# Kernel optimization log

Hardware: AMD Instinct MI355X
Metric: run time of the kernel (lower is better)

## Reference

```python
import jax, jax.numpy as jnp
import numpy as np

H, HK, D = 16, 4, 128          # query heads, kv heads, head_dim
HID, INTER = 2048, 8192        # hidden_size, intermediate_size
L, N_UND = 4096, 3072          # total packed len (sum(sample_lens)), num und tokens
SAMPLE_LENS = [2048, 2048]
EPS = 1e-6


def rmsnorm(x, w, eps=EPS):
    v = jnp.mean(jnp.square(x), axis=-1, keepdims=True)
    return x * jax.lax.rsqrt(v + eps) * w


def setup_inputs() -> dict:
    key = jax.random.key(0)
    ks = jax.random.split(key, 12)
    x = jax.random.normal(ks[0], (N_UND, HID), jnp.float32)
    und_idx = jnp.sort(jax.random.permutation(ks[1], L)[:N_UND]).astype(jnp.int64)
    # RoPE tables (source computes RoPE but its attention consumes pre-RoPE tensors)
    pos = jnp.arange(L, dtype=jnp.float32)
    inv_freq = 1.0 / (10000.0 ** (jnp.arange(0, D, 2, dtype=jnp.float32) / D))
    ang = pos[:, None] * inv_freq[None, :]
    cos = jnp.concatenate([jnp.cos(ang), jnp.cos(ang)], axis=-1)
    sin = jnp.concatenate([jnp.sin(ang), jnp.sin(ang)], axis=-1)
    # block-diagonal causal mask over packed sequence (one causal block per sample)
    offs = np.cumsum([0] + SAMPLE_LENS)
    m = np.zeros((L, L), dtype=bool)
    for a, b in zip(offs[:-1], offs[1:]):
        m[a:b, a:b] = np.tril(np.ones((b - a, b - a), dtype=bool))
    mask = jnp.asarray(m)
    w = lambda k, shape: jax.random.normal(k, shape, jnp.float32) * 0.02
    return dict(
        packed_sequence=x, und_idx=und_idx, cos=cos, sin=sin, mask=mask,
        Wq=w(ks[2], (H * D, HID)), bq=w(ks[3], (H * D,)),
        Wk=w(ks[4], (HK * D, HID)), bk=w(ks[5], (HK * D,)),
        Wv=w(ks[6], (HK * D, HID)), bv=w(ks[7], (HK * D,)),
        Wo=w(ks[8], (HID, H * D)),
        q_norm_w=jnp.ones((D,), jnp.float32), k_norm_w=jnp.ones((D,), jnp.float32),
        ln1_w=jnp.ones((HID,), jnp.float32), ln2_w=jnp.ones((HID,), jnp.float32),
        Wg=w(ks[9], (INTER, HID)), Wu=w(ks[10], (INTER, HID)), Wd=w(ks[11], (HID, INTER)),
    )


def reference(packed_sequence, und_idx, cos, sin, mask, Wq, bq, Wk, bk, Wv, bv, Wo,
              q_norm_w, k_norm_w, ln1_w, ln2_w, Wg, Wu, Wd):
    G = H // HK  # num_key_value_groups
    resid = packed_sequence
    x = rmsnorm(packed_sequence, ln1_w)
    # projections on und tokens only, then scatter into zero-initialized packed tensors
    q = (x @ Wq.T + bq).reshape(-1, H, D)
    k = (x @ Wk.T + bk).reshape(-1, HK, D)
    v = (x @ Wv.T + bv).reshape(-1, HK, D)
    Q = jnp.zeros((L, H, D), x.dtype).at[und_idx].set(q)
    K = jnp.zeros((L, HK, D), x.dtype).at[und_idx].set(k)
    V = jnp.zeros((L, HK, D), x.dtype).at[und_idx].set(v)
    # QK RMSNorm (zero rows stay zero, matching scatter-of-normed-und-rows)
    Q = rmsnorm(Q, q_norm_w)
    K = rmsnorm(K, k_norm_w)
    # NOTE: the source applies apply_rotary_pos_emb(Q, K, cos, sin) but both attention
    # branches consume the pre-RoPE normed tensors, so RoPE has no effect; we mirror that.
    Kx = jnp.repeat(K, G, axis=1)  # [L, H, D] GQA expand (each kv head repeated G times)
    Vx = jnp.repeat(V, G, axis=1)
    scores = jnp.einsum('qhd,khd->hqk', Q, Kx) / jnp.sqrt(jnp.asarray(D, x.dtype))
    scores = jnp.where(mask[None], scores, jnp.finfo(scores.dtype).min)
    attn = jax.nn.softmax(scores, axis=-1)
    ctx = jnp.einsum('hqk,khd->qhd', attn, Vx).reshape(L, H * D)
    attn_out = ctx[und_idx] @ Wo.T
    h = resid + attn_out
    y = rmsnorm(h, ln2_w)
    mlp = (jax.nn.silu(y @ Wg.T) * (y @ Wu.T)) @ Wd.T
    return h + mlp
```

## Files before the change

kernel.cpp:

```cpp
#include <hip/hip_runtime.h>
#include <math.h>


#define NU     3072
#define LPACK  4096
#define HIDN   2048
#define QKV_LD 3072
#define EPSF   1e-6f

typedef unsigned short u16;
typedef unsigned int   u32;
typedef __attribute__((ext_vector_type(8)))  __bf16 bf16x8;
typedef __attribute__((ext_vector_type(4)))  float  f32x4;
typedef __attribute__((ext_vector_type(16))) float  f32x16;

union FRAG { uint4 q; u16 u[8]; bf16x8 b; };

__device__ __forceinline__ u16 f2bf(float f) {
    u32 u = __float_as_uint(f);
    u32 r = (u + 0x7fffu + ((u >> 16) & 1u)) >> 16;
    return (u16)r;
}
__device__ __forceinline__ float bf2f(u16 h) {
    return __uint_as_float(((u32)h) << 16);
}
__device__ __forceinline__ void gload_lds16(const u16* g, u16* lds) {
    __builtin_amdgcn_global_load_lds(
        (const __attribute__((address_space(1))) u32*)g,
        (__attribute__((address_space(3))) u32*)lds, 16, 0, 0);
}


__global__ __launch_bounds__(256) void inv_init_kernel(int* __restrict__ inv) {
    inv[blockIdx.x * 256 + threadIdx.x] = -1;
}
__global__ __launch_bounds__(256) void inv_set_kernel(const int* __restrict__ und,
                                                      int* __restrict__ inv) {
    int i = blockIdx.x * 256 + threadIdx.x;
    inv[und[i]] = i;
}


struct CvtArgs {
    const float* src[7];
    u16*         dst[7];
    int          n8[7];
};

__global__ __launch_bounds__(256) void cvt_all_kernel(CvtArgs a) {
    int seg = blockIdx.y;
    const float* in = a.src[seg];
    u16* out = a.dst[seg];
    int n8 = a.n8[seg];
    int idx = blockIdx.x * 256 + threadIdx.x;
    int stride = gridDim.x * 256;
    for (int i = idx; i < n8; i += stride) {
        float4 va = *(const float4*)(in + (size_t)i * 8);
        float4 vb = *(const float4*)(in + (size_t)i * 8 + 4);
        FRAG f;
        f.u[0] = f2bf(va.x); f.u[1] = f2bf(va.y); f.u[2] = f2bf(va.z); f.u[3] = f2bf(va.w);
        f.u[4] = f2bf(vb.x); f.u[5] = f2bf(vb.y); f.u[6] = f2bf(vb.z); f.u[7] = f2bf(vb.w);
        *(uint4*)(out + (size_t)i * 8) = f.q;
    }
}


__global__ __launch_bounds__(256) void rmsnorm_bf16_kernel(const float* __restrict__ in,
                                                           const float* __restrict__ w,
                                                           u16* __restrict__ out) {
    int row = blockIdx.x;
    const float4* p = (const float4*)(in + (size_t)row * HIDN);
    float4 a = p[threadIdx.x * 2];
    float4 b = p[threadIdx.x * 2 + 1];
    float ss = a.x*a.x + a.y*a.y + a.z*a.z + a.w*a.w
             + b.x*b.x + b.y*b.y + b.z*b.z + b.w*b.w;
    #pragma unroll
    for (int off = 32; off > 0; off >>= 1) ss += __shfl_xor(ss, off, 64);
    __shared__ float red[4];
    if ((threadIdx.x & 63) == 0) red[threadIdx.x >> 6] = ss;
    __syncthreads();
    float tot = red[0] + red[1] + red[2] + red[3];
    float sc  = rsqrtf(tot * (1.0f / HIDN) + EPSF);
    const float4* wp = (const float4*)w;
    float4 w0 = wp[threadIdx.x * 2], w1 = wp[threadIdx.x * 2 + 1];
    FRAG f;
    f.u[0] = f2bf(a.x*sc*w0.x); f.u[1] = f2bf(a.y*sc*w0.y);
    f.u[2] = f2bf(a.z*sc*w0.z); f.u[3] = f2bf(a.w*sc*w0.w);
    f.u[4] = f2bf(b.x*sc*w1.x); f.u[5] = f2bf(b.y*sc*w1.y);
    f.u[6] = f2bf(b.z*sc*w1.z); f.u[7] = f2bf(b.w*sc*w1.w);
    *(uint4*)(out + (size_t)row * HIDN + threadIdx.x * 8) = f.q;
}


__global__ __launch_bounds__(64) void qnorm_kernel(u16* __restrict__ qkv,
                                                   const float* __restrict__ w) {
    int i = blockIdx.x, h = blockIdx.y, t = threadIdx.x;
    u16* p = qkv + (size_t)i * QKV_LD + h * 128 + t * 2;
    u32 pr = *(u32*)p;
    float x0 = bf2f((u16)(pr & 0xffff)), x1 = bf2f((u16)(pr >> 16));
    float ss = x0*x0 + x1*x1;
    #pragma unroll
    for (int off = 32; off > 0; off >>= 1) ss += __shfl_xor(ss, off, 64);
    float sc = rsqrtf(ss * (1.0f / 128.f) + EPSF);
    float2 wv = *(const float2*)(w + t * 2);
    u32 res = (u32)f2bf(x0*sc*wv.x) | ((u32)f2bf(x1*sc*wv.y) << 16);
    *(u32*)p = res;
}


__global__ __launch_bounds__(64) void scatter_kv_kernel(const u16* __restrict__ qkvb,
                                                        const int* __restrict__ inv,
                                                        const float* __restrict__ knw,
                                                        u16* __restrict__ Kb,
                                                        u16* __restrict__ Vb) {
    int l = blockIdx.x, hkk = blockIdx.y, t = threadIdx.x;
    int i = inv[l];
    size_t off = (size_t)l * 512 + hkk * 128 + t * 2;
    if (i < 0) {
        *(u32*)(Kb + off) = 0u;
        *(u32*)(Vb + off) = 0u;
        return;
    }
    const u16* kp = qkvb + (size_t)i * QKV_LD + 2048 + hkk * 128 + t * 2;
    u32 kv = *(const u32*)kp;
    float k0 = bf2f((u16)(kv & 0xffff)), k1 = bf2f((u16)(kv >> 16));
    float ss = k0*k0 + k1*k1;
    #pragma unroll
    for (int off2 = 32; off2 > 0; off2 >>= 1) ss += __shfl_xor(ss, off2, 64);
    float sc = rsqrtf(ss * (1.0f / 128.f) + EPSF);
    float2 wv = *(const float2*)(knw + t * 2);
    u32 res = (u32)f2bf(k0*sc*wv.x) | ((u32)f2bf(k1*sc*wv.y) << 16);
    *(u32*)(Kb + off) = res;
    const u16* vp = qkvb + (size_t)i * QKV_LD + 2560 + hkk * 128 + t * 2;
    *(u32*)(Vb + off) = *(const u32*)vp;
}


template <int MODE>
__global__ __launch_bounds__(256, 2) void gemm_bf16_kernel(
        const u16* __restrict__ A, int lda,
        const u16* __restrict__ B0, const u16* __restrict__ B1, const u16* __restrict__ B2,
        int n1, int n2, int ldb,
        const float* __restrict__ bias0, const float* __restrict__ bias1,
        const float* __restrict__ bias2,
        const float* __restrict__ addend,
        void* __restrict__ Cout, int ldc, int K)
{
    __shared__ u16 As[128 * 64];
    __shared__ u16 Bs[128 * 64];
    const int tid = threadIdx.x;
    const int w = tid >> 6, lane = tid & 63;
    const int m0 = blockIdx.y * 128, n0 = blockIdx.x * 128;
    const u16* Bp; const float* bias; int nb;
    if (n0 < n1)      { Bp = B0; bias = bias0; nb = n0; }
    else if (n0 < n2) { Bp = B1; bias = bias1; nb = n0 - n1; }
    else              { Bp = B2; bias = bias2; nb = n0 - n2; }
    const int wr = w >> 1, wc = w & 1;
    const int cl = lane & 15, kg = lane >> 4;

    f32x4 acc[4][4];
    #pragma unroll
    for (int i = 0; i < 4; ++i)
        #pragma unroll
        for (int j = 0; j < 4; ++j)
            #pragma unroll
            for (int r = 0; r < 4; ++r) acc[i][j][r] = 0.f;

    for (int k0 = 0; k0 < K; k0 += 64) {
        #pragma unroll
        for (int j = 0; j < 4; ++j) {
            int slot = j * 256 + tid;
            int row = slot >> 3, jp = slot & 7;
            int j2 = jp ^ (row & 7);
            gload_lds16(A + (size_t)(m0 + row) * lda + k0 + j2 * 8,
                        &As[(j * 256 + w * 64) * 8]);
        }
        #pragma unroll
        for (int j = 0; j < 4; ++j) {
            int slot = j * 256 + tid;
            int row = slot >> 3, jp = slot & 7;
            int j2 = jp ^ (row & 7);
            gload_lds16(Bp + (size_t)(nb + row) * ldb + k0 + j2 * 8,
                        &Bs[(j * 256 + w * 64) * 8]);
        }
        __syncthreads();
        #pragma unroll
        for (int ks = 0; ks < 2; ++ks) {
            FRAG af[4], bfr[4];
            #pragma unroll
            for (int mi = 0; mi < 4; ++mi) {
                int row = wr * 64 + mi * 16 + cl;
                int dblk = ks * 4 + kg;
                af[mi].q = *(const uint4*)&As[row * 64 + ((dblk ^ (row & 7)) * 8)];
            }
            #pragma unroll
            for (int ni = 0; ni < 4; ++ni) {
                int row = wc * 64 + ni * 16 + cl;
                int dblk = ks * 4 + kg;
                bfr[ni].q = *(const uint4*)&Bs[row * 64 + ((dblk ^ (row & 7)) * 8)];
            }
            #pragma unroll
            for (int mi = 0; mi < 4; ++mi)
                #pragma unroll
                for (int ni = 0; ni < 4; ++ni)
                    acc[mi][ni] = __builtin_amdgcn_mfma_f32_16x16x32_bf16(
                        af[mi].b, bfr[ni].b, acc[mi][ni], 0, 0, 0);
        }
        __syncthreads();
    }
    #pragma unroll
    for (int mi = 0; mi < 4; ++mi) {
        #pragma unroll
        for (int ni = 0; ni < 4; ++ni) {
            int gcol = n0 + wc * 64 + ni * 16 + cl;
            float bv = 0.f;
            if (MODE == 0) bv = bias[nb + wc * 64 + ni * 16 + cl];
            #pragma unroll
            for (int r = 0; r < 4; ++r) {
                int grow = m0 + wr * 64 + mi * 16 + kg * 4 + r;
                float v = acc[mi][ni][r] + bv;
                if (MODE == 0) {
                    ((u16*)Cout)[(size_t)grow * ldc + gcol] = f2bf(v);
                } else {
                    v += addend[(size_t)grow * ldc + gcol];
                    ((float*)Cout)[(size_t)grow * ldc + gcol] = v;
                }
            }
        }
    }
}


__global__ __launch_bounds__(256, 2) void gemm_gateup_bf16_kernel(
        const u16* __restrict__ A,
        const u16* __restrict__ Bg, const u16* __restrict__ Bu,
        u16* __restrict__ act, int ldc)
{
    __shared__ u16 As[128 * 64];
    __shared__ u16 Gs[128 * 64];
    __shared__ u16 Us[128 * 64];
    const int tid = threadIdx.x;
    const int w = tid >> 6, lane = tid & 63;
    const int m0 = blockIdx.y * 128, n0 = blockIdx.x * 128;
    const int wr = w >> 1, wc = w & 1;
    const int cl = lane & 15, kg = lane >> 4;

    f32x4 ag[4][4], au[4][4];
    #pragma unroll
    for (int i = 0; i < 4; ++i)
        #pragma unroll
        for (int j = 0; j < 4; ++j)
            #pragma unroll
            for (int r = 0; r < 4; ++r) { ag[i][j][r] = 0.f; au[i][j][r] = 0.f; }

    for (int k0 = 0; k0 < HIDN; k0 += 64) {
        #pragma unroll
        for (int j = 0; j < 4; ++j) {
            int slot = j * 256 + tid;
            int row = slot >> 3, jp = slot & 7;
            int j2 = jp ^ (row & 7);
            gload_lds16(A + (size_t)(m0 + row) * HIDN + k0 + j2 * 8,
                        &As[(j * 256 + w * 64) * 8]);
            gload_lds16(Bg + (size_t)(n0 + row) * HIDN + k0 + j2 * 8,
                        &Gs[(j * 256 + w * 64) * 8]);
            gload_lds16(Bu + (size_t)(n0 + row) * HIDN + k0 + j2 * 8,
                        &Us[(j * 256 + w * 64) * 8]);
        }
        __syncthreads();
        #pragma unroll
        for (int ks = 0; ks < 2; ++ks) {
            FRAG af[4], gf[4], uf[4];
            #pragma unroll
            for (int mi = 0; mi < 4; ++mi) {
                int row = wr * 64 + mi * 16 + cl;
                int dblk = ks * 4 + kg;
                af[mi].q = *(const uint4*)&As[row * 64 + ((dblk ^ (row & 7)) * 8)];
            }
            #pragma unroll
            for (int ni = 0; ni < 4; ++ni) {
                int row = wc * 64 + ni * 16 + cl;
                int dblk = ks * 4 + kg;
                gf[ni].q = *(const uint4*)&Gs[row * 64 + ((dblk ^ (row & 7)) * 8)];
                uf[ni].q = *(const uint4*)&Us[row * 64 + ((dblk ^ (row & 7)) * 8)];
            }
            #pragma unroll
            for (int mi = 0; mi < 4; ++mi)
                #pragma unroll
                for (int ni = 0; ni < 4; ++ni) {
                    ag[mi][ni] = __builtin_amdgcn_mfma_f32_16x16x32_bf16(
                        af[mi].b, gf[ni].b, ag[mi][ni], 0, 0, 0);
                    au[mi][ni] = __builtin_amdgcn_mfma_f32_16x16x32_bf16(
                        af[mi].b, uf[ni].b, au[mi][ni], 0, 0, 0);
                }
        }
        __syncthreads();
    }
    #pragma unroll
    for (int mi = 0; mi < 4; ++mi) {
        #pragma unroll
        for (int ni = 0; ni < 4; ++ni) {
            int gcol = n0 + wc * 64 + ni * 16 + cl;
            #pragma unroll
            for (int r = 0; r < 4; ++r) {
                int grow = m0 + wr * 64 + mi * 16 + kg * 4 + r;
                float g = ag[mi][ni][r], u = au[mi][ni][r];
                float s = g / (1.f + __expf(-g));
                act[(size_t)grow * ldc + gcol] = f2bf(s * u);
            }
        }
    }
}


__global__ __launch_bounds__(256, 2) void attn_mfma_kernel(
        const u16* __restrict__ qkv,
        const u16* __restrict__ Kb,
        const u16* __restrict__ Vb,
        const int* __restrict__ und,
        u16* __restrict__ ctxb)
{
    const int h = blockIdx.y, hk = h >> 2;
    const int i0 = blockIdx.x * 128;
    const int tid = threadIdx.x;
    const int w = tid >> 6, lane = tid & 63;
    const int ql = lane & 31, hi = lane >> 5;

    __shared__ __align__(16) unsigned char SM[36864];
    u16*  Kt = (u16*)SM;
    u16*  Vt = (u16*)(SM + 16384);
    float* Ot = (float*)SM;

    const int iq  = i0 + w * 32 + ql;
    const int pqv = und[iq];
    const int rsv = pqv & ~2047;
    const int kend_w = __shfl(pqv, 31, 64);
    const int kbeg_w = __shfl(pqv, 0, 64) & ~2047;
    const int kbeg_b = und[i0] & ~2047;
    const int kend_b = und[i0 + 127];
    const int nt = ((kend_b - kbeg_b) >> 5) + 1;

    FRAG qf[8];
    const u16* qbase = qkv + (size_t)iq * QKV_LD + h * 128;
    #pragma unroll
    for (int ds = 0; ds < 8; ++ds)
        qf[ds].q = *(const uint4*)(qbase + ds * 16 + hi * 8);

    f32x16 Oa[4];
    #pragma unroll
    for (int dg = 0; dg < 4; ++dg)
        #pragma unroll
        for (int r = 0; r < 16; ++r) Oa[dg][r] = 0.f;
    float m_run = -1e30f, l_run = 0.f;
    const float SCALE = 0.08838834764831845f;

    const int kp = tid & 15, d0 = (tid >> 4) * 8;

    FRAG vr0, vr1;
    {
        #pragma unroll
        for (int j = 0; j < 2; ++j) {
            int sb = (j * 4 + w) * 64;
            int slot = sb + lane;
            int r = slot >> 4, jp = slot & 15;
            int jj = jp ^ (r & 15);
            gload_lds16(Kb + (size_t)(kbeg_b + r) * 512 + hk * 128 + jj * 8,
                        &Kt[sb * 8]);
        }
        const u16* v0 = Vb + (size_t)(kbeg_b + kp * 2) * 512 + hk * 128 + d0;
        vr0.q = *(const uint4*)v0;
        vr1.q = *(const uint4*)(v0 + 512);
    }

    for (int t = 0; t < nt; ++t) {
        const int cur = t & 1;
        const int k0 = kbeg_b + t * 32;
        #pragma unroll
        for (int i = 0; i < 8; ++i) {
            u32 val = (u32)vr0.u[i] | ((u32)vr1.u[i] << 16);
            *(u32*)&Vt[cur * 5120 + (d0 + i) * 40 + kp * 2] = val;
        }
        __syncthreads();
        if (t + 1 < nt) {
            int kn = k0 + 32;
            #pragma unroll
            for (int j = 0; j < 2; ++j) {
                int sb = (j * 4 + w) * 64;
                int slot = sb + lane;
                int r = slot >> 4, jp = slot & 15;
                int jj = jp ^ (r & 15);
                gload_lds16(Kb + (size_t)(kn + r) * 512 + hk * 128 + jj * 8,
                            &Kt[(cur ^ 1) * 4096 + sb * 8]);
            }
            const u16* v0 = Vb + (size_t)(kn + kp * 2) * 512 + hk * 128 + d0;
            vr0.q = *(const uint4*)v0;
            vr1.q = *(const uint4*)(v0 + 512);
        }
        if (k0 + 31 >= kbeg_w && k0 <= kend_w) {
            f32x16 st;
            #pragma unroll
            for (int r = 0; r < 16; ++r) st[r] = 0.f;
            __builtin_amdgcn_s_setprio(1);
            #pragma unroll
            for (int ds = 0; ds < 8; ++ds) {
                FRAG kf;
                kf.q = *(const uint4*)&Kt[cur * 4096 + ql * 128 +
                                          (((ds * 2 + hi) ^ (ql & 15)) * 8)];
                st = __builtin_amdgcn_mfma_f32_32x32x16_bf16(kf.b, qf[ds].b, st, 0, 0, 0);
            }
            __builtin_amdgcn_s_setprio(0);
            float p[16];
            float mloc = -1e30f;
            #pragma unroll
            for (int r = 0; r < 16; ++r) {
                int key = k0 + (r & 3) + ((r >> 2) << 3) + (hi << 2);
                float s = (key >= rsv && key <= pqv) ? st[r] * SCALE : -1e30f;
                p[r] = s;
                mloc = fmaxf(mloc, s);
            }
            float mfull = fmaxf(mloc, __shfl_xor(mloc, 32, 64));
            float mnew = fmaxf(m_run, mfull);
            float corr = __expf(m_run - mnew);
            float psum = 0.f;
            #pragma unroll
            for (int r = 0; r < 16; ++r) {
                float e = (p[r] > -1e29f) ? __expf(p[r] - mnew) : 0.f;
                p[r] = e; psum += e;
            }
            psum += __shfl_xor(psum, 32, 64);
            l_run = l_run * corr + psum;
            if (__any(mnew > m_run)) {
                #pragma unroll
                for (int r = 0; r < 16; ++r) {
                    float cr = __shfl(corr, (r & 3) + ((r >> 2) << 3) + (hi << 2), 64);
                    #pragma unroll
                    for (int dg = 0; dg < 4; ++dg) Oa[dg][r] *= cr;
                }
            }
            m_run = mnew;
            u32 pa[2][4];
            #pragma unroll
            for (int s = 0; s < 2; ++s) {
                #pragma unroll
                for (int t2 = 0; t2 < 2; ++t2) {
                    u32 a = (u32)f2bf(p[8*s + 2*t2]) | ((u32)f2bf(p[8*s + 2*t2 + 1]) << 16);
                    u32 b = (u32)f2bf(p[8*s + 4 + 2*t2]) | ((u32)f2bf(p[8*s + 4 + 2*t2 + 1]) << 16);
                    asm volatile("v_permlane32_swap_b32 %0, %1" : "+v"(a), "+v"(b));
                    pa[s][t2] = a; pa[s][t2 + 2] = b;
                }
            }
            __builtin_amdgcn_s_setprio(1);
            #pragma unroll
            for (int s = 0; s < 2; ++s) {
                FRAG pau;
                pau.q = make_uint4(pa[s][0], pa[s][1], pa[s][2], pa[s][3]);
                #pragma unroll
                for (int dg = 0; dg < 4; ++dg) {
                    FRAG vf;
                    vf.q = *(const uint4*)&Vt[cur * 5120 + (dg * 32 + ql) * 40 +
                                              s * 16 + hi * 8];
                    Oa[dg] = __builtin_amdgcn_mfma_f32_32x32x16_bf16(pau.b, vf.b, Oa[dg], 0, 0, 0);
                }
            }
            __builtin_amdgcn_s_setprio(0);
        }
    }
    __syncthreads();

    float linv = 1.f / l_run;
    #pragma unroll
    for (int dg = 0; dg < 4; ++dg) {
        #pragma unroll
        for (int r = 0; r < 16; ++r)
            Ot[w * 1152 + ((r & 3) + ((r >> 2) << 3) + (hi << 2)) * 36 + ql] = Oa[dg][r];
        __syncthreads();
        float4 v0 = *(const float4*)&Ot[w * 1152 + ql * 36 + hi * 16 + 0];
        float4 v1 = *(const float4*)&Ot[w * 1152 + ql * 36 + hi * 16 + 4];
        float4 v2 = *(const float4*)&Ot[w * 1152 + ql * 36 + hi * 16 + 8];
        float4 v3 = *(const float4*)&Ot[w * 1152 + ql * 36 + hi * 16 + 12];
        FRAG a, b;
        a.u[0] = f2bf(v0.x * linv); a.u[1] = f2bf(v0.y * linv);
        a.u[2] = f2bf(v0.z * linv); a.u[3] = f2bf(v0.w * linv);
        a.u[4] = f2bf(v1.x * linv); a.u[5] = f2bf(v1.y * linv);
        a.u[6] = f2bf(v1.z * linv); a.u[7] = f2bf(v1.w * linv);
        b.u[0] = f2bf(v2.x * linv); b.u[1] = f2bf(v2.y * linv);
        b.u[2] = f2bf(v2.z * linv); b.u[3] = f2bf(v2.w * linv);
        b.u[4] = f2bf(v3.x * linv); b.u[5] = f2bf(v3.y * linv);
        b.u[6] = f2bf(v3.z * linv); b.u[7] = f2bf(v3.w * linv);
        u16* dst = ctxb + (size_t)(i0 + w * 32 + ql) * HIDN + h * 128 + dg * 32 + hi * 16;
        *(uint4*)dst = a.q;
        *(uint4*)(dst + 8) = b.q;
        __syncthreads();
    }
}


extern "C" void kernel_launch(void* const* d_in, const int* in_sizes, int n_in,
                              void* d_out, int out_size, void* d_ws, size_t ws_size,
                              hipStream_t stream) {
    const float* x    = (const float*)d_in[0];
    const int*   und  = (const int*)d_in[1];
    const float* Wq  = (const float*)d_in[5];
    const float* bq  = (const float*)d_in[6];
    const float* Wk  = (const float*)d_in[7];
    const float* bk  = (const float*)d_in[8];
    const float* Wv  = (const float*)d_in[9];
    const float* bv  = (const float*)d_in[10];
    const float* Wo  = (const float*)d_in[11];
    const float* qnw = (const float*)d_in[12];
    const float* knw = (const float*)d_in[13];
    const float* ln1 = (const float*)d_in[14];
    const float* ln2 = (const float*)d_in[15];
    const float* Wg  = (const float*)d_in[16];
    const float* Wu  = (const float*)d_in[17];
    const float* Wd  = (const float*)d_in[18];
    float* out = (float*)d_out;

    char* W = (char*)d_ws;
    u16* WqB = (u16*)(W + 0);
    u16* WkB = (u16*)(W + 8388608);
    u16* WvB = (u16*)(W + 10485760);
    u16* WoB = (u16*)(W + 12582912);
    u16* WgB = (u16*)(W + 20971520);
    u16* WuB = (u16*)(W + 54525952);
    u16* WdB = (u16*)(W + 88080384);
    char* R1 = W + 121634816;
    u16* qkvb = (u16*)R1;
    u16* ctxb = (u16*)(R1 + 18874368);
    u16* acth = (u16*)R1;
    float* hbuf = (float*)(W + 153092096);
    u16* xnb = (u16*)(W + 178257920);
    u16* Kbf = xnb;
    u16* Vbf = (u16*)(W + 178257920 + 4194304);
    u16* ynb = xnb;
    int* inv = (int*)(W + 190840832);

    const int BIG = 1 << 30;

    inv_init_kernel<<<16, 256, 0, stream>>>(inv);
    inv_set_kernel<<<12, 256, 0, stream>>>(und, inv);

    CvtArgs ca;
    ca.src[0] = Wq; ca.dst[0] = WqB; ca.n8[0] = 524288;
    ca.src[1] = Wk; ca.dst[1] = WkB; ca.n8[1] = 131072;
    ca.src[2] = Wv; ca.dst[2] = WvB; ca.n8[2] = 131072;
    ca.src[3] = Wo; ca.dst[3] = WoB; ca.n8[3] = 524288;
    ca.src[4] = Wg; ca.dst[4] = WgB; ca.n8[4] = 2097152;
    ca.src[5] = Wu; ca.dst[5] = WuB; ca.n8[5] = 2097152;
    ca.src[6] = Wd; ca.dst[6] = WdB; ca.n8[6] = 2097152;
    cvt_all_kernel<<<dim3(1024, 7), 256, 0, stream>>>(ca);

    rmsnorm_bf16_kernel<<<NU, 256, 0, stream>>>(x, ln1, xnb);
    gemm_bf16_kernel<0><<<dim3(24, 24), 256, 0, stream>>>(
        xnb, 2048, WqB, WkB, WvB, 2048, 2560, 2048,
        bq, bk, bv, nullptr, qkvb, QKV_LD, 2048);
    qnorm_kernel<<<dim3(NU, 16), 64, 0, stream>>>(qkvb, qnw);
    scatter_kv_kernel<<<dim3(LPACK, 4), 64, 0, stream>>>(qkvb, inv, knw, Kbf, Vbf);
    attn_mfma_kernel<<<dim3(24, 16), 256, 0, stream>>>(qkvb, Kbf, Vbf, und, ctxb);
    gemm_bf16_kernel<1><<<dim3(16, 24), 256, 0, stream>>>(
        ctxb, 2048, WoB, WoB, WoB, BIG, BIG, 2048,
        nullptr, nullptr, nullptr, x, hbuf, 2048, 2048);
    rmsnorm_bf16_kernel<<<NU, 256, 0, stream>>>(hbuf, ln2, ynb);
    gemm_gateup_bf16_kernel<<<dim3(32, 24), 256, 0, stream>>>(
        ynb, WgB, WuB, acth, 4096);
    gemm_bf16_kernel<1><<<dim3(16, 24), 256, 0, stream>>>(
        acth, 4096, WdB, WdB, WdB, BIG, BIG, 8192,
        nullptr, nullptr, nullptr, hbuf, out, 2048, 4096);
    gemm_gateup_bf16_kernel<<<dim3(32, 24), 256, 0, stream>>>(
        ynb, WgB + (size_t)4096 * 2048, WuB + (size_t)4096 * 2048, acth, 4096);
    gemm_bf16_kernel<1><<<dim3(16, 24), 256, 0, stream>>>(
        acth, 4096, WdB + 4096, WdB, WdB, BIG, BIG, 8192,
        nullptr, nullptr, nullptr, out, out, 2048, 4096);
}
```

Baseline: 733.2 us.

## Restructure attention to single-wave blocks with register-fed K and pre-transposed V

Attention now launches one 64-thread wave per 32 queries instead of 256-thread blocks per 128 queries. K and V fragments are loaded straight from global memory into registers, with next-tile prefetch, in place of LDS staging and __syncthreads. A new vtrans_kernel writes V pre-transposed (d-major) so each lane can load V fragments contiguously. The softmax switches to exp2 with a folded log2e scale, skips rescaling while the running max grows by at most 8, and converts with v_cvt_pk_bf16_f32. The cost is an extra kernel launch plus a transpose pass, more registers per lane, and K/V tiles re-read from global/L2 by each wave rather than shared across the block.

After: 736.4 us. About the same (+0.4%).

```diff
diff --git a/kernel.cpp b/kernel.cpp
--- a/kernel.cpp
+++ b/kernel.cpp
@@ -108,17 +108,15 @@
 }
 
 
-__global__ __launch_bounds__(64) void scatter_kv_kernel(const u16* __restrict__ qkvb,
-                                                        const int* __restrict__ inv,
-                                                        const float* __restrict__ knw,
-                                                        u16* __restrict__ Kb,
-                                                        u16* __restrict__ Vb) {
+__global__ __launch_bounds__(64) void scatter_k_kernel(const u16* __restrict__ qkvb,
+                                                       const int* __restrict__ inv,
+                                                       const float* __restrict__ knw,
+                                                       u16* __restrict__ Kb) {
     int l = blockIdx.x, hkk = blockIdx.y, t = threadIdx.x;
     int i = inv[l];
     size_t off = (size_t)l * 512 + hkk * 128 + t * 2;
     if (i < 0) {
         *(u32*)(Kb + off) = 0u;
-        *(u32*)(Vb + off) = 0u;
         return;
     }
     const u16* kp = qkvb + (size_t)i * QKV_LD + 2048 + hkk * 128 + t * 2;
@@ -131,8 +129,37 @@
     float2 wv = *(const float2*)(knw + t * 2);
     u32 res = (u32)f2bf(k0*sc*wv.x) | ((u32)f2bf(k1*sc*wv.y) << 16);
     *(u32*)(Kb + off) = res;
-    const u16* vp = qkvb + (size_t)i * QKV_LD + 2560 + hkk * 128 + t * 2;
-    *(u32*)(Vb + off) = *(const u32*)vp;
+}
+
+
+__global__ __launch_bounds__(256) void vtrans_kernel(const u16* __restrict__ qkvb,
+                                                     const int* __restrict__ inv,
+                                                     u16* __restrict__ VT) {
+    int hk = blockIdx.y, l0 = blockIdx.x * 64;
+    int tid = threadIdx.x;
+    __shared__ u16 T[64][136];
+    {
+        int k = tid >> 2, cg = (tid & 3) * 32;
+        int i = inv[l0 + k];
+        #pragma unroll
+        for (int j = 0; j < 4; ++j) {
+            uint4 v = make_uint4(0u, 0u, 0u, 0u);
+            if (i >= 0)
+                v = *(const uint4*)(qkvb + (size_t)i * QKV_LD + 2560 + hk * 128 + cg + j * 8);
+            *(uint4*)&T[k][cg + j * 8] = v;
+        }
+    }
+    __syncthreads();
+    int d = tid >> 1, hf = tid & 1;
+    FRAG o[4];
+    #pragma unroll
+    for (int j = 0; j < 4; ++j)
+        #pragma unroll
+        for (int e = 0; e < 8; ++e)
+            o[j].u[e] = T[hf * 32 + j * 8 + e][d];
+    u16* dst = VT + ((size_t)hk * 128 + d) * 4096 + l0 + hf * 32;
+    #pragma unroll
+    for (int j = 0; j < 4; ++j) *(uint4*)(dst + j * 8) = o[j].q;
 }
 
 
@@ -312,32 +339,26 @@
 }
 
 
-__global__ __launch_bounds__(256, 2) void attn_mfma_kernel(
+__global__ __launch_bounds__(64, 2) void attn_mfma_kernel(
         const u16* __restrict__ qkv,
         const u16* __restrict__ Kb,
-        const u16* __restrict__ Vb,
+        const u16* __restrict__ VT,
         const int* __restrict__ und,
         u16* __restrict__ ctxb)
 {
     const int h = blockIdx.y, hk = h >> 2;
-    const int i0 = blockIdx.x * 128;
-    const int tid = threadIdx.x;
-    const int w = tid >> 6, lane = tid & 63;
+    const int i0 = blockIdx.x * 32;
+    const int lane = threadIdx.x;
     const int ql = lane & 31, hi = lane >> 5;
 
-    __shared__ __align__(16) unsigned char SM[36864];
-    u16*  Kt = (u16*)SM;
-    u16*  Vt = (u16*)(SM + 16384);
-    float* Ot = (float*)SM;
-
-    const int iq  = i0 + w * 32 + ql;
+    __shared__ float Ot[32][36];
+
+    const int iq  = i0 + ql;
     const int pqv = und[iq];
     const int rsv = pqv & ~2047;
-    const int kend_w = __shfl(pqv, 31, 64);
-    const int kbeg_w = __shfl(pqv, 0, 64) & ~2047;
-    const int kbeg_b = und[i0] & ~2047;
-    const int kend_b = und[i0 + 127];
-    const int nt = ((kend_b - kbeg_b) >> 5) + 1;
+    const int kend = __shfl(pqv, 31, 64);
+    const int kbeg = __shfl(pqv, 0, 64) & ~2047;
+    const int nt = ((kend - kbeg) >> 5) + 1;
 
     FRAG qf[8];
     const u16* qbase = qkv + (size_t)iq * QKV_LD + h * 128;
@@ -345,138 +366,123 @@
     for (int ds = 0; ds < 8; ++ds)
         qf[ds].q = *(const uint4*)(qbase + ds * 16 + hi * 8);
 
+    const u16* vbase = VT + ((size_t)hk * 128 + ql) * 4096 + hi * 8;
+
     f32x16 Oa[4];
     #pragma unroll
     for (int dg = 0; dg < 4; ++dg)
         #pragma unroll
         for (int r = 0; r < 16; ++r) Oa[dg][r] = 0.f;
     float m_run = -1e30f, l_run = 0.f;
-    const float SCALE = 0.08838834764831845f;
-
-    const int kp = tid & 15, d0 = (tid >> 4) * 8;
-
-    FRAG vr0, vr1;
+    const float SC2 = 0.12752764f;
+
+    FRAG kf[8], kn[8], vf[8];
     {
-        #pragma unroll
-        for (int j = 0; j < 2; ++j) {
-            int sb = (j * 4 + w) * 64;
-            int slot = sb + lane;
-            int r = slot >> 4, jp = slot & 15;
-            int jj = jp ^ (r & 15);
-            gload_lds16(Kb + (size_t)(kbeg_b + r) * 512 + hk * 128 + jj * 8,
-                        &Kt[sb * 8]);
-        }
-        const u16* v0 = Vb + (size_t)(kbeg_b + kp * 2) * 512 + hk * 128 + d0;
-        vr0.q = *(const uint4*)v0;
-        vr1.q = *(const uint4*)(v0 + 512);
+        const u16* kr = Kb + (size_t)(kbeg + ql) * 512 + hk * 128 + hi * 8;
+        #pragma unroll
+        for (int ds = 0; ds < 8; ++ds)
+            kf[ds].q = *(const uint4*)(kr + ds * 16);
+        #pragma unroll
+        for (int s = 0; s < 2; ++s)
+            #pragma unroll
+            for (int dg = 0; dg < 4; ++dg)
+                vf[s * 4 + dg].q = *(const uint4*)(vbase + (size_t)(dg * 32) * 4096 +
+                                                   kbeg + s * 16);
     }
 
     for (int t = 0; t < nt; ++t) {
-        const int cur = t & 1;
-        const int k0 = kbeg_b + t * 32;
-        #pragma unroll
-        for (int i = 0; i < 8; ++i) {
-            u32 val = (u32)vr0.u[i] | ((u32)vr1.u[i] << 16);
-            *(u32*)&Vt[cur * 5120 + (d0 + i) * 40 + kp * 2] = val;
-        }
-        __syncthreads();
+        const int k0 = kbeg + t * 32;
+        f32x16 st;
+        #pragma unroll
+        for (int r = 0; r < 16; ++r) st[r] = 0.f;
+        __builtin_amdgcn_s_setprio(1);
+        #pragma unroll
+        for (int ds = 0; ds < 8; ++ds)
+            st = __builtin_amdgcn_mfma_f32_32x32x16_bf16(kf[ds].b, qf[ds].b, st, 0, 0, 0);
+        __builtin_amdgcn_s_setprio(0);
         if (t + 1 < nt) {
-            int kn = k0 + 32;
-            #pragma unroll
-            for (int j = 0; j < 2; ++j) {
-                int sb = (j * 4 + w) * 64;
-                int slot = sb + lane;
-                int r = slot >> 4, jp = slot & 15;
-                int jj = jp ^ (r & 15);
-                gload_lds16(Kb + (size_t)(kn + r) * 512 + hk * 128 + jj * 8,
-                            &Kt[(cur ^ 1) * 4096 + sb * 8]);
-            }
-            const u16* v0 = Vb + (size_t)(kn + kp * 2) * 512 + hk * 128 + d0;
-            vr0.q = *(const uint4*)v0;
-            vr1.q = *(const uint4*)(v0 + 512);
-        }
-        if (k0 + 31 >= kbeg_w && k0 <= kend_w) {
-            f32x16 st;
-            #pragma unroll
-            for (int r = 0; r < 16; ++r) st[r] = 0.f;
-            __builtin_amdgcn_s_setprio(1);
-            #pragma unroll
-            for (int ds = 0; ds < 8; ++ds) {
-                FRAG kf;
-                kf.q = *(const uint4*)&Kt[cur * 4096 + ql * 128 +
-                                          (((ds * 2 + hi) ^ (ql & 15)) * 8)];
-                st = __builtin_amdgcn_mfma_f32_32x32x16_bf16(kf.b, qf[ds].b, st, 0, 0, 0);
-            }
-            __builtin_amdgcn_s_setprio(0);
-            float p[16];
-            float mloc = -1e30f;
+            const u16* kr = Kb + (size_t)(k0 + 32 + ql) * 512 + hk * 128 + hi * 8;
+            #pragma unroll
+            for (int ds = 0; ds < 8; ++ds)
+                kn[ds].q = *(const uint4*)(kr + ds * 16);
+        }
+        float p[16];
+        float mloc = -1e30f;
+        #pragma unroll
+        for (int r = 0; r < 16; ++r) {
+            int key = k0 + (r & 3) + ((r >> 2) << 3) + (hi << 2);
+            float s = (key >= rsv && key <= pqv) ? st[r] * SC2 : -1e30f;
+            p[r] = s;
+            mloc = fmaxf(mloc, s);
+        }
+        float pm = fmaxf(mloc, __shfl_xor(mloc, 32, 64));
+        if (!__all(pm - m_run <= 8.f)) {
+            float mnew = fmaxf(m_run, pm);
+            float corr = exp2f(m_run - mnew);
+            l_run *= corr;
             #pragma unroll
             for (int r = 0; r < 16; ++r) {
-                int key = k0 + (r & 3) + ((r >> 2) << 3) + (hi << 2);
-                float s = (key >= rsv && key <= pqv) ? st[r] * SCALE : -1e30f;
-                p[r] = s;
-                mloc = fmaxf(mloc, s);
-            }
-            float mfull = fmaxf(mloc, __shfl_xor(mloc, 32, 64));
-            float mnew = fmaxf(m_run, mfull);
-            float corr = __expf(m_run - mnew);
-            float psum = 0.f;
-            #pragma unroll
-            for (int r = 0; r < 16; ++r) {
-                float e = (p[r] > -1e29f) ? __expf(p[r] - mnew) : 0.f;
-                p[r] = e; psum += e;
-            }
-            psum += __shfl_xor(psum, 32, 64);
-            l_run = l_run * corr + psum;
-            if (__any(mnew > m_run)) {
+                float cr = __shfl(corr, (r & 3) + ((r >> 2) << 3) + (hi << 2), 64);
                 #pragma unroll
-                for (int r = 0; r < 16; ++r) {
-                    float cr = __shfl(corr, (r & 3) + ((r >> 2) << 3) + (hi << 2), 64);
-                    #pragma unroll
-                    for (int dg = 0; dg < 4; ++dg) Oa[dg][r] *= cr;
-                }
+                for (int dg = 0; dg < 4; ++dg) Oa[dg][r] *= cr;
             }
             m_run = mnew;
-            u32 pa[2][4];
-            #pragma unroll
-            for (int s = 0; s < 2; ++s) {
+        }
+        float psum = 0.f;
+        #pragma unroll
+        for (int r = 0; r < 16; ++r) {
+            float e = (p[r] > -1e29f) ? exp2f(p[r] - m_run) : 0.f;
+            p[r] = e; psum += e;
+        }
+        psum += __shfl_xor(psum, 32, 64);
+        l_run += psum;
+        u32 pa[2][4];
+        #pragma unroll
+        for (int s = 0; s < 2; ++s) {
+            #pragma unroll
+            for (int t2 = 0; t2 < 2; ++t2) {
+                u32 a, b;
+                asm volatile("v_cvt_pk_bf16_f32 %0, %1, %2"
+                             : "=v"(a) : "v"(p[8*s + 2*t2]), "v"(p[8*s + 2*t2 + 1]));
+                asm volatile("v_cvt_pk_bf16_f32 %0, %1, %2"
+                             : "=v"(b) : "v"(p[8*s + 4 + 2*t2]), "v"(p[8*s + 4 + 2*t2 + 1]));
+                asm volatile("v_permlane32_swap_b32 %0, %1" : "+v"(a), "+v"(b));
+                pa[s][t2] = a; pa[s][t2 + 2] = b;
+            }
+        }
+        __builtin_amdgcn_s_setprio(1);
+        #pragma unroll
+        for (int s = 0; s < 2; ++s) {
+            FRAG pau;
+            pau.q = make_uint4(pa[s][0], pa[s][1], pa[s][2], pa[s][3]);
+            #pragma unroll
+            for (int dg = 0; dg < 4; ++dg)
+                Oa[dg] = __builtin_amdgcn_mfma_f32_32x32x16_bf16(
+                    pau.b, vf[s * 4 + dg].b, Oa[dg], 0, 0, 0);
+        }
+        __builtin_amdgcn_s_setprio(0);
+        if (t + 1 < nt) {
+            #pragma unroll
+            for (int s = 0; s < 2; ++s)
                 #pragma unroll
-                for (int t2 = 0; t2 < 2; ++t2) {
-                    u32 a = (u32)f2bf(p[8*s + 2*t2]) | ((u32)f2bf(p[8*s + 2*t2 + 1]) << 16);
-                    u32 b = (u32)f2bf(p[8*s + 4 + 2*t2]) | ((u32)f2bf(p[8*s + 4 + 2*t2 + 1]) << 16);
-                    asm volatile("v_permlane32_swap_b32 %0, %1" : "+v"(a), "+v"(b));
-                    pa[s][t2] = a; pa[s][t2 + 2] = b;
-                }
-            }
-            __builtin_amdgcn_s_setprio(1);
-            #pragma unroll
-            for (int s = 0; s < 2; ++s) {
-                FRAG pau;
-                pau.q = make_uint4(pa[s][0], pa[s][1], pa[s][2], pa[s][3]);
-                #pragma unroll
-                for (int dg = 0; dg < 4; ++dg) {
-                    FRAG vf;
-                    vf.q = *(const uint4*)&Vt[cur * 5120 + (dg * 32 + ql) * 40 +
-                                              s * 16 + hi * 8];
-                    Oa[dg] = __builtin_amdgcn_mfma_f32_32x32x16_bf16(pau.b, vf.b, Oa[dg], 0, 0, 0);
-                }
-            }
-            __builtin_amdgcn_s_setprio(0);
-        }
-    }
-    __syncthreads();
+                for (int dg = 0; dg < 4; ++dg)
+                    vf[s * 4 + dg].q = *(const uint4*)(vbase + (size_t)(dg * 32) * 4096 +
+                                                       k0 + 32 + s * 16);
+            #pragma unroll
+            for (int ds = 0; ds < 8; ++ds) kf[ds] = kn[ds];
+        }
+    }
 
     float linv = 1.f / l_run;
     #pragma unroll
     for (int dg = 0; dg < 4; ++dg) {
         #pragma unroll
         for (int r = 0; r < 16; ++r)
-            Ot[w * 1152 + ((r & 3) + ((r >> 2) << 3) + (hi << 2)) * 36 + ql] = Oa[dg][r];
-        __syncthreads();
-        float4 v0 = *(const float4*)&Ot[w * 1152 + ql * 36 + hi * 16 + 0];
-        float4 v1 = *(const float4*)&Ot[w * 1152 + ql * 36 + hi * 16 + 4];
-        float4 v2 = *(const float4*)&Ot[w * 1152 + ql * 36 + hi * 16 + 8];
-        float4 v3 = *(const float4*)&Ot[w * 1152 + ql * 36 + hi * 16 + 12];
+            Ot[(r & 3) + ((r >> 2) << 3) + (hi << 2)][ql] = Oa[dg][r];
+        float4 v0 = *(const float4*)&Ot[ql][hi * 16 + 0];
+        float4 v1 = *(const float4*)&Ot[ql][hi * 16 + 4];
+        float4 v2 = *(const float4*)&Ot[ql][hi * 16 + 8];
+        float4 v3 = *(const float4*)&Ot[ql][hi * 16 + 12];
         FRAG a, b;
         a.u[0] = f2bf(v0.x * linv); a.u[1] = f2bf(v0.y * linv);
         a.u[2] = f2bf(v0.z * linv); a.u[3] = f2bf(v0.w * linv);
@@ -486,10 +492,9 @@
         b.u[2] = f2bf(v2.z * linv); b.u[3] = f2bf(v2.w * linv);
         b.u[4] = f2bf(v3.x * linv); b.u[5] = f2bf(v3.y * linv);
         b.u[6] = f2bf(v3.z * linv); b.u[7] = f2bf(v3.w * linv);
-        u16* dst = ctxb + (size_t)(i0 + w * 32 + ql) * HIDN + h * 128 + dg * 32 + hi * 16;
+        u16* dst = ctxb + (size_t)(i0 + ql) * HIDN + h * 128 + dg * 32 + hi * 16;
         *(uint4*)dst = a.q;
         *(uint4*)(dst + 8) = b.q;
-        __syncthreads();
     }
 }
 
@@ -530,7 +535,7 @@
     float* hbuf = (float*)(W + 153092096);
     u16* xnb = (u16*)(W + 178257920);
     u16* Kbf = xnb;
-    u16* Vbf = (u16*)(W + 178257920 + 4194304);
+    u16* VTb = (u16*)(W + 178257920 + 4194304);
     u16* ynb = xnb;
     int* inv = (int*)(W + 190840832);
 
@@ -554,8 +559,9 @@
         xnb, 2048, WqB, WkB, WvB, 2048, 2560, 2048,
         bq, bk, bv, nullptr, qkvb, QKV_LD, 2048);
     qnorm_kernel<<<dim3(NU, 16), 64, 0, stream>>>(qkvb, qnw);
-    scatter_kv_kernel<<<dim3(LPACK, 4), 64, 0, stream>>>(qkvb, inv, knw, Kbf, Vbf);
-    attn_mfma_kernel<<<dim3(24, 16), 256, 0, stream>>>(qkvb, Kbf, Vbf, und, ctxb);
+    scatter_k_kernel<<<dim3(LPACK, 4), 64, 0, stream>>>(qkvb, inv, knw, Kbf);
+    vtrans_kernel<<<dim3(64, 4), 256, 0, stream>>>(qkvb, inv, VTb);
+    attn_mfma_kernel<<<dim3(96, 16), 64, 0, stream>>>(qkvb, Kbf, VTb, und, ctxb);
     gemm_bf16_kernel<1><<<dim3(16, 24), 256, 0, stream>>>(
         ctxb, 2048, WoB, WoB, WoB, BIG, BIG, 2048,
         nullptr, nullptr, nullptr, x, hbuf, 2048, 2048);
```
